# Kernel optimization log

Measured on AMD Instinct MI355X. Metric: run time of the kernel, lower is better.

## Reference

```python
import jax, jax.numpy as jnp
import numpy as np

N, DX, DS, NLAB, NSMAT = 20000, 16, 64, 10, 64
E_HALF = 160000
E = 2 * E_HALF
N_LABELED = 2000
N_HIDDEN = 6  # six Linear(nsmat,nsmat) layers between input and output layers


def setup_inputs() -> dict:
    key = jax.random.key(0)
    ks = jax.random.split(key, 16)
    xembed = jax.random.normal(ks[0], (N, DX), jnp.float32)
    sembed = jax.random.normal(ks[1], (N, DS), jnp.float32)
    # ylprob are log-probabilities (original uses exp(ylprob) in the KL term)
    ylprob = jax.nn.log_softmax(jax.random.normal(ks[2], (N, NLAB), jnp.float32), axis=1)
    # build edge list with explicit reverse pairs so loss_orth is exercised
    s_half = jax.random.randint(ks[3], (E_HALF,), 0, N, jnp.int32)
    t_half = jax.random.randint(ks[4], (E_HALF,), 0, N, jnp.int32)
    src = jnp.concatenate([s_half, t_half])
    tgt = jnp.concatenate([t_half, s_half])
    edge_w = jax.random.uniform(ks[5], (E,), jnp.float32, 0.1, 1.0)
    rev1 = jnp.arange(E_HALF, dtype=jnp.int32)
    rev2 = rev1 + E_HALF
    idvert = jax.random.randint(ks[6], (N_LABELED,), 0, N, jnp.int32)
    fcW_in = jax.random.normal(ks[7], (2 * DS, NSMAT), jnp.float32) / np.sqrt(2 * DS)
    fcb_in = jnp.zeros((NSMAT,), jnp.float32)
    fcW_h = jax.random.normal(ks[8], (N_HIDDEN, NSMAT, NSMAT), jnp.float32) / np.sqrt(NSMAT)
    fcb_h = jnp.zeros((N_HIDDEN, NSMAT), jnp.float32)
    fcW_out = jax.random.normal(ks[9], (NSMAT, DX * DX), jnp.float32) / np.sqrt(NSMAT)
    fcb_out = jnp.zeros((DX * DX,), jnp.float32)
    # cl_smat params: Linear(dimx, nlab) + LogSoftmax
    clW = jax.random.normal(ks[10], (DX, NLAB), jnp.float32) / np.sqrt(DX)
    clb = jnp.zeros((NLAB,), jnp.float32)
    return dict(xembed=xembed, sembed=sembed, ylprob=ylprob, edge_w=edge_w,
                fcW_in=fcW_in, fcb_in=fcb_in, fcW_h=fcW_h, fcb_h=fcb_h,
                fcW_out=fcW_out, fcb_out=fcb_out, clW=clW, clb=clb,
                src=src, tgt=tgt, rev1=rev1, rev2=rev2, idvert=idvert)


def _edge_matrices(sf, tf, fcW_in, fcb_in, fcW_h, fcb_h, fcW_out, fcb_out):
    # [E, 2*dims] -> 8-layer ReLU MLP -> [E, dimx, dimx]
    h = jax.nn.relu(jnp.concatenate([sf, tf], axis=1) @ fcW_in + fcb_in)
    for i in range(N_HIDDEN):
        h = jax.nn.relu(h @ fcW_h[i] + fcb_h[i])
    return (h @ fcW_out + fcb_out).reshape(-1, DX, DX)


def reference(xembed, sembed, ylprob, edge_w, fcW_in, fcb_in, fcW_h, fcb_h,
              fcW_out, fcb_out, clW, clb, src, tgt, rev1, rev2, idvert):
    # per-edge sheaf transport matrices from gathered structure embeddings
    edge_mats = _edge_matrices(sembed[src], sembed[tgt],
                               fcW_in, fcb_in, fcW_h, fcb_h, fcW_out, fcb_out)

    # orthogonality loss over reverse edge pairs: mean RMS(A@B - I) * dimx
    prod = jnp.einsum('eij,ejk->eik', edge_mats[rev1], edge_mats[rev2])
    diff = prod - jnp.eye(DX, dtype=prod.dtype)
    loss_orth = jnp.mean(jnp.sqrt(jnp.mean(diff * diff, axis=(1, 2)) * (DX * DX)))

    # message passing: gather -> bmm -> weighted scatter-add -> degree normalize
    messages = jnp.einsum('eij,ej->ei', edge_mats, xembed[src])  # [E, dimx]
    weighted = messages * edge_w[:, None]
    new_x = jax.ops.segment_sum(weighted, tgt, num_segments=N)   # [N, dimx]
    deg = jax.ops.segment_sum(edge_w, tgt, num_segments=N)       # [N]
    xmaped = jnp.where((deg > 0)[:, None], new_x / jnp.maximum(deg, 1e-20)[:, None], new_x)

    loss_smap = jnp.mean((xmaped - xembed) ** 2) * DX

    # KL(y || g) on labeled nodes; cl_smat = Linear + LogSoftmax
    glprob = jax.nn.log_softmax(xmaped[idvert] @ clW + clb, axis=1)
    ylp = ylprob[idvert]
    loss_lbpr = jnp.mean(jnp.sum(jnp.exp(ylp) * (ylp - glprob), axis=1))

    # original recomputes the same MLP on the same inputs and takes the MSE of
    # two identical tensors -> exactly zero (and zero gradient)
    loss_cons = jnp.zeros((), xembed.dtype)

    return (loss_orth, loss_cons, loss_smap, loss_lbpr)
```

## Files before the change

### kernel.cpp

```cpp
#include <hip/hip_runtime.h>
#include <hip/hip_bf16.h>

#define N_NODES   20000
#define DX        16
#define DS        64
#define NLAB      10
#define NSMAT     64
#define E_HALF    160000
#define E_TOT     320000
#define N_LABELED 2000
#define N_HIDDEN  6

#define PAIRS 32
#define NT    (E_HALF / PAIRS)

typedef short bf16x8 __attribute__((ext_vector_type(8)));
typedef float f32x4  __attribute__((ext_vector_type(4)));
#define MFMA16(a, b, c) __builtin_amdgcn_mfma_f32_16x16x32_bf16((a), (b), (c), 0, 0, 0)

#define LDS_A0    0
#define LDS_H0    16384
#define LDS_H1    24576
#define LDS_MT    32768
#define LDS_X     49152
#define LDS_BH    51200
#define LDS_BOUT  52736
#define LDS_TOTAL 53760

#define WS_W0     0
#define WS_WH     16384
#define WS_WOUT   65536
#define WS_FLOATS 98304

__device__ __forceinline__ unsigned short f2bf(float f) {
    unsigned int u = __float_as_uint(f);
    unsigned int r = (u + 0x7fffu + ((u >> 16) & 1u)) >> 16;
    return (unsigned short)r;
}
__device__ __forceinline__ unsigned int packbf(float a, float b) {
    return (unsigned int)f2bf(a) | ((unsigned int)f2bf(b) << 16);
}
__device__ __forceinline__ float bflo(unsigned int u) { return __uint_as_float(u << 16); }
__device__ __forceinline__ float bfhi(unsigned int u) { return __uint_as_float(u & 0xffff0000u); }

__global__ void k_prep(const float* __restrict__ Win, const float* __restrict__ Wh,
                       const float* __restrict__ Wout, unsigned short* __restrict__ wsw) {
    const int idx = blockIdx.x * 256 + threadIdx.x;
    if (idx >= 49152) return;
    float val; int base, KK, k, n;
    if (idx < 8192) {
        k = idx >> 6; n = idx & 63; val = Win[idx]; base = WS_W0 / 2; KK = 4;
    } else if (idx < 32768) {
        const int r = idx - 8192; const int l = r >> 12; const int rr = r & 4095;
        k = rr >> 6; n = rr & 63; val = Wh[r]; base = (WS_WH + l * 8192) / 2; KK = 2;
    } else {
        const int r = idx - 32768; k = r >> 8; n = r & 255;
        val = Wout[r]; base = WS_WOUT / 2; KK = 2;
    }
    const int ntile = n >> 4, kk = k >> 5, hi = (k >> 3) & 3, j = k & 7;
    const int lane = hi * 16 + (n & 15);
    wsw[base + (((ntile * KK + kk) * 64 + lane) * 8 + j)] = f2bf(val);
}

__global__ void k_zero(float* __restrict__ p, int n) {
    int i = blockIdx.x * blockDim.x + threadIdx.x;
    const int stride = gridDim.x * blockDim.x;
    for (; i < n; i += stride) p[i] = 0.0f;
}

__global__ __launch_bounds__(256, 3) void k_main(
    const float* __restrict__ xembed, const float* __restrict__ sembed,
    const float* __restrict__ edge_w,
    const float* __restrict__ bin, const float* __restrict__ bh,
    const float* __restrict__ bout,
    const int* __restrict__ src, const int* __restrict__ tgt,
    const unsigned short* __restrict__ wsw,
    float* __restrict__ newx, float* __restrict__ deg,
    float* __restrict__ orth_part)
{
    extern __shared__ char lds[];
    const int tid    = threadIdx.x;
    const int lane   = tid & 63;
    const int wv     = tid >> 6;
    const int lane15 = lane & 15;
    const int hi     = lane >> 4;
    const int p0     = blockIdx.x * PAIRS;

    if (tid < 96)       ((float4*)(lds + LDS_BH))[tid]       = ((const float4*)bh)[tid];
    else if (tid < 160) ((float4*)(lds + LDS_BOUT))[tid - 96] = ((const float4*)bout)[tid - 96];

    {
        const int si = tid >> 3, sc = tid & 7;
        const bool sT = (sc >= 4); const int scc = sc & 3;
        const int p = p0 + si;
        const int nodeA = sT ? tgt[p] : src[p];
        const float4* nrow = (const float4*)(sembed + (size_t)nodeA * DS + scc * 16);
        const float4 v0 = nrow[0], v1 = nrow[1], v2 = nrow[2], v3 = nrow[3];
        const int colA = (sT ? 128 : 0) + scc * 32;
        const int colB = (sT ? 0 : 128) + scc * 32;
        const int sXor = (si & 7) << 4;
        uint2 pk;
        pk.x = packbf(v0.x, v0.y); pk.y = packbf(v0.z, v0.w);
        *(uint2*)(lds + LDS_A0 + si * 256 + ((colA + 0) ^ sXor)) = pk;
        *(uint2*)(lds + LDS_A0 + (32 + si) * 256 + ((colB + 0) ^ sXor)) = pk;
        pk.x = packbf(v1.x, v1.y); pk.y = packbf(v1.z, v1.w);
        *(uint2*)(lds + LDS_A0 + si * 256 + ((colA + 8) ^ sXor)) = pk;
        *(uint2*)(lds + LDS_A0 + (32 + si) * 256 + ((colB + 8) ^ sXor)) = pk;
        pk.x = packbf(v2.x, v2.y); pk.y = packbf(v2.z, v2.w);
        *(uint2*)(lds + LDS_A0 + si * 256 + ((colA + 16) ^ sXor)) = pk;
        *(uint2*)(lds + LDS_A0 + (32 + si) * 256 + ((colB + 16) ^ sXor)) = pk;
        pk.x = packbf(v3.x, v3.y); pk.y = packbf(v3.z, v3.w);
        *(uint2*)(lds + LDS_A0 + si * 256 + ((colA + 24) ^ sXor)) = pk;
        *(uint2*)(lds + LDS_A0 + (32 + si) * 256 + ((colB + 24) ^ sXor)) = pk;

        const int sed = tid >> 2, sqq = tid & 3;
        const int nodeX = (sed < 32) ? src[p0 + sed] : tgt[p0 + sed - 32];
        const float4 vx = *(const float4*)(xembed + (size_t)nodeX * DX + sqq * 4);
        pk.x = packbf(vx.x, vx.y); pk.y = packbf(vx.z, vx.w);
        *(uint2*)(lds + LDS_X + sed * 32 + sqq * 8) = pk;
    }

    float bin_r[4];
    #pragma unroll
    for (int n = 0; n < 4; ++n) bin_r[n] = bin[16 * n + lane15];

    const int arow = 16 * wv + lane15;
    const int axor = (arow & 7) << 4;

    __syncthreads();

    {
        bf16x8 a[4];
        #pragma unroll
        for (int kk = 0; kk < 4; ++kk)
            a[kk] = *(const bf16x8*)(lds + LDS_A0 + arow * 256 + ((kk * 64 + hi * 16) ^ axor));
        const unsigned short* w0g = wsw + WS_W0 / 2;
        #pragma unroll
        for (int n = 0; n < 4; ++n) {
            f32x4 acc = {bin_r[n], bin_r[n], bin_r[n], bin_r[n]};
            #pragma unroll
            for (int kk = 0; kk < 4; ++kk) {
                const bf16x8 b = *(const bf16x8*)(w0g + ((n * 4 + kk) * 64 + lane) * 8);
                acc = MFMA16(a[kk], b, acc);
            }
            #pragma unroll
            for (int r = 0; r < 4; ++r) {
                const int row = 16 * wv + 4 * hi + r;
                *(unsigned short*)(lds + LDS_H0 + row * 128 +
                    (((16 * n + lane15) * 2) ^ ((row & 7) << 4))) = f2bf(fmaxf(acc[r], 0.0f));
            }
        }
    }
    __syncthreads();

    #pragma unroll
    for (int l = 0; l < 6; ++l) {
        const int sB = (l & 1) ? LDS_H1 : LDS_H0;
        const int dB = (l & 1) ? LDS_H0 : LDS_H1;
        const unsigned short* whg = wsw + WS_WH / 2 + l * 4096;
        const bf16x8 a0 = *(const bf16x8*)(lds + sB + arow * 128 + ((hi * 16) ^ axor));
        const bf16x8 a1 = *(const bf16x8*)(lds + sB + arow * 128 + ((64 + hi * 16) ^ axor));
        #pragma unroll
        for (int n = 0; n < 4; ++n) {
            const float bv = ((const float*)(lds + LDS_BH))[l * 64 + 16 * n + lane15];
            f32x4 acc = {bv, bv, bv, bv};
            const bf16x8 b0 = *(const bf16x8*)(whg + ((n * 2 + 0) * 64 + lane) * 8);
            const bf16x8 b1 = *(const bf16x8*)(whg + ((n * 2 + 1) * 64 + lane) * 8);
            acc = MFMA16(a0, b0, acc);
            acc = MFMA16(a1, b1, acc);
            #pragma unroll
            for (int r = 0; r < 4; ++r) {
                const int row = 16 * wv + 4 * hi + r;
                *(unsigned short*)(lds + dB + row * 128 +
                    (((16 * n + lane15) * 2) ^ ((row & 7) << 4))) = f2bf(fmaxf(acc[r], 0.0f));
            }
        }
    }

    {
        const bf16x8 a0 = *(const bf16x8*)(lds + LDS_H0 + arow * 128 + ((hi * 16) ^ axor));
        const bf16x8 a1 = *(const bf16x8*)(lds + LDS_H0 + arow * 128 + ((64 + hi * 16) ^ axor));
        const unsigned short* wog = wsw + WS_WOUT / 2;
        #pragma unroll
        for (int n = 0; n < 16; ++n) {
            const float bv = ((const float*)(lds + LDS_BOUT))[16 * n + lane15];
            const bf16x8 b0 = *(const bf16x8*)(wog + ((n * 2 + 0) * 64 + lane) * 8);
            const bf16x8 b1 = *(const bf16x8*)(wog + ((n * 2 + 1) * 64 + lane) * 8);
            f32x4 acc = {bv, bv, bv, bv};
            acc = MFMA16(a0, b0, acc);
            acc = MFMA16(a1, b1, acc);
            #pragma unroll
            for (int r = 0; r < 4; ++r) {
                const int row = 16 * wv + 4 * hi + r;
                const unsigned short mv = f2bf(acc[r]);
                if (wv < 2) {
                    const int i = row;
                    *(unsigned short*)(lds + LDS_A0 + i * 512 +
                        (((n * 16 + lane15) * 2) ^ ((i & 7) << 4))) = mv;
                } else {
                    const int i = row - 32;
                    *(unsigned short*)(lds + LDS_MT + i * 512 +
                        (((lane15 * 16 + n) * 2) ^ ((i & 7) << 4))) = mv;
                }
            }
        }
    }
    __syncthreads();

    {
        const int e = tid >> 2, q = tid & 3;
        const int i = e & 31;
        const bool isB = (e >= 32);
        const uint4 x0 = *(const uint4*)(lds + LDS_X + e * 32);
        const uint4 x1 = *(const uint4*)(lds + LDS_X + e * 32 + 16);
        float xv[16];
        xv[0]  = bflo(x0.x); xv[1]  = bfhi(x0.x); xv[2]  = bflo(x0.y); xv[3]  = bfhi(x0.y);
        xv[4]  = bflo(x0.z); xv[5]  = bfhi(x0.z); xv[6]  = bflo(x0.w); xv[7]  = bfhi(x0.w);
        xv[8]  = bflo(x1.x); xv[9]  = bfhi(x1.x); xv[10] = bflo(x1.y); xv[11] = bfhi(x1.y);
        xv[12] = bflo(x1.z); xv[13] = bfhi(x1.z); xv[14] = bflo(x1.w); xv[15] = bfhi(x1.w);
        const int p = p0 + i;
        const float w_e  = isB ? edge_w[p + E_HALF] : edge_w[p];
        const int target = isB ? src[p] : tgt[p];
        const int ixor = (i & 7) << 4;
        if (!isB) {
            #pragma unroll
            for (int jj = 0; jj < 4; ++jj) {
                const int row = 4 * q + jj;
                const uint4 m0 = *(const uint4*)(lds + LDS_A0 + i * 512 + ((row * 32) ^ ixor));
                const uint4 m1 = *(const uint4*)(lds + LDS_A0 + i * 512 + ((row * 32 + 16) ^ ixor));
                float m = bflo(m0.x) * xv[0];
                m = fmaf(bfhi(m0.x), xv[1], m);  m = fmaf(bflo(m0.y), xv[2], m);
                m = fmaf(bfhi(m0.y), xv[3], m);  m = fmaf(bflo(m0.z), xv[4], m);
                m = fmaf(bfhi(m0.z), xv[5], m);  m = fmaf(bflo(m0.w), xv[6], m);
                m = fmaf(bfhi(m0.w), xv[7], m);  m = fmaf(bflo(m1.x), xv[8], m);
                m = fmaf(bfhi(m1.x), xv[9], m);  m = fmaf(bflo(m1.y), xv[10], m);
                m = fmaf(bfhi(m1.y), xv[11], m); m = fmaf(bflo(m1.z), xv[12], m);
                m = fmaf(bfhi(m1.z), xv[13], m); m = fmaf(bflo(m1.w), xv[14], m);
                m = fmaf(bfhi(m1.w), xv[15], m);
                atomicAdd(&newx[(size_t)target * DX + row], w_e * m);
            }
        } else {
            float macc[4] = {0.f, 0.f, 0.f, 0.f};
            #pragma unroll
            for (int c = 0; c < 16; ++c) {
                const uint2 v = *(const uint2*)(lds + LDS_MT + i * 512 + ((c * 32 + q * 8) ^ ixor));
                const float xc = xv[c];
                macc[0] = fmaf(bflo(v.x), xc, macc[0]);
                macc[1] = fmaf(bfhi(v.x), xc, macc[1]);
                macc[2] = fmaf(bflo(v.y), xc, macc[2]);
                macc[3] = fmaf(bfhi(v.y), xc, macc[3]);
            }
            #pragma unroll
            for (int jj = 0; jj < 4; ++jj)
                atomicAdd(&newx[(size_t)target * DX + 4 * q + jj], w_e * macc[jj]);
        }
        if (q == 0) atomicAdd(&deg[target], w_e);
    }

    float wsum = 0.0f;
    {
        const bf16x8 zf = {0, 0, 0, 0, 0, 0, 0, 0};
        #pragma unroll
        for (int pp = 0; pp < 8; ++pp) {
            const int pi = 8 * wv + pp;
            const int pxor = (pi & 7) << 4;
            const int off = (lane15 * 32 + (hi & 1) * 16) ^ pxor;
            bf16x8 af  = *(const bf16x8*)(lds + LDS_A0 + pi * 512 + off);
            bf16x8 bfr = *(const bf16x8*)(lds + LDS_MT + pi * 512 + off);
            if (hi >= 2) { af = zf; bfr = zf; }
            f32x4 pr = {0.f, 0.f, 0.f, 0.f};
            pr = MFMA16(af, bfr, pr);
            float ss = 0.0f;
            #pragma unroll
            for (int r = 0; r < 4; ++r) {
                const float d = pr[r] - ((4 * hi + r == lane15) ? 1.0f : 0.0f);
                ss = fmaf(d, d, ss);
            }
            #pragma unroll
            for (int o = 32; o > 0; o >>= 1) ss += __shfl_xor(ss, o, 64);
            wsum += sqrtf(ss);
        }
    }
    __syncthreads();
    if (lane == 0) ((float*)(lds + LDS_BH))[wv] = wsum;
    __syncthreads();
    if (tid == 0) {
        const float* pw = (const float*)(lds + LDS_BH);
        atomicAdd(&orth_part[blockIdx.x & 255], pw[0] + pw[1] + pw[2] + pw[3]);
    }
}

__device__ __forceinline__ float block_reduce_256(float v) {
    __shared__ float part[4];
    #pragma unroll
    for (int off = 32; off > 0; off >>= 1) v += __shfl_xor(v, off, 64);
    const int lane = threadIdx.x & 63, wid = threadIdx.x >> 6;
    if (lane == 0) part[wid] = v;
    __syncthreads();
    float s = 0.0f;
    if (threadIdx.x == 0) {
        #pragma unroll
        for (int i = 0; i < 4; ++i) s += part[i];
    }
    return s;
}

__global__ __launch_bounds__(256) void k_smap(
    const float* __restrict__ xembed, float* __restrict__ nx,
    const float* __restrict__ deg, float* __restrict__ accum)
{
    const int n = blockIdx.x * 256 + threadIdx.x;
    float ss = 0.0f;
    if (n < N_NODES) {
        const float d = deg[n];
        const float inv = 1.0f / fmaxf(d, 1e-20f);
        #pragma unroll
        for (int c = 0; c < DX; ++c) {
            const float v  = nx[(size_t)n * DX + c];
            const float xm = (d > 0.0f) ? v * inv : v;
            nx[(size_t)n * DX + c] = xm;
            const float df = xm - xembed[(size_t)n * DX + c];
            ss = fmaf(df, df, ss);
        }
    }
    ss = block_reduce_256(ss);
    if (threadIdx.x == 0) atomicAdd(&accum[1], ss);
}

__global__ __launch_bounds__(256) void k_lbpr(
    const float* __restrict__ ylprob, const float* __restrict__ xmaped,
    const float* __restrict__ clW, const float* __restrict__ clb,
    const int* __restrict__ idvert, float* __restrict__ accum)
{
    const int v = blockIdx.x * 256 + threadIdx.x;
    float kl = 0.0f;
    if (v < N_LABELED) {
        const int n = idvert[v];
        float z[NLAB];
        #pragma unroll
        for (int c = 0; c < NLAB; ++c) z[c] = clb[c];
        #pragma unroll
        for (int i = 0; i < DX; ++i) {
            const float xi = xmaped[(size_t)n * DX + i];
            #pragma unroll
            for (int c = 0; c < NLAB; ++c) z[c] = fmaf(xi, clW[i * NLAB + c], z[c]);
        }
        float mx = z[0];
        #pragma unroll
        for (int c = 1; c < NLAB; ++c) mx = fmaxf(mx, z[c]);
        float se = 0.0f;
        #pragma unroll
        for (int c = 0; c < NLAB; ++c) se += expf(z[c] - mx);
        const float lse = mx + logf(se);
        #pragma unroll
        for (int c = 0; c < NLAB; ++c) {
            const float yl = ylprob[(size_t)n * NLAB + c];
            kl += expf(yl) * (yl - (z[c] - lse));
        }
    }
    kl = block_reduce_256(kl);
    if (threadIdx.x == 0) atomicAdd(&accum[2], kl);
}

__global__ __launch_bounds__(256) void k_final(
    const float* __restrict__ accum, const float* __restrict__ orth_part,
    float* __restrict__ out)
{
    float v = orth_part[threadIdx.x];
    v = block_reduce_256(v);
    if (threadIdx.x == 0) {
        out[0] = v * (1.0f / (float)E_HALF);
        out[1] = 0.0f;
        out[2] = accum[1] * (1.0f / (float)N_NODES);
        out[3] = accum[2] * (1.0f / (float)N_LABELED);
    }
}

extern "C" void kernel_launch(void* const* d_in, const int* in_sizes, int n_in,
                              void* d_out, int out_size, void* d_ws, size_t ws_size,
                              hipStream_t stream) {
    const float* xembed = (const float*)d_in[0];
    const float* sembed = (const float*)d_in[1];
    const float* ylprob = (const float*)d_in[2];
    const float* edge_w = (const float*)d_in[3];
    const float* Win    = (const float*)d_in[4];
    const float* bin    = (const float*)d_in[5];
    const float* Wh     = (const float*)d_in[6];
    const float* bh     = (const float*)d_in[7];
    const float* Wout   = (const float*)d_in[8];
    const float* bout   = (const float*)d_in[9];
    const float* clW    = (const float*)d_in[10];
    const float* clb    = (const float*)d_in[11];
    const int*   src    = (const int*)d_in[12];
    const int*   tgt    = (const int*)d_in[13];
    const int*   idvert = (const int*)d_in[16];

    unsigned short* wsw = (unsigned short*)d_ws;
    float* wsF       = (float*)((char*)d_ws + WS_FLOATS);
    float* newx      = wsF;
    float* deg       = wsF + (size_t)N_NODES * DX;
    float* accum     = deg + N_NODES;
    float* orth_part = accum + 4;
    const int nzero = N_NODES * DX + N_NODES + 4 + 256;

    k_prep<<<192, 256, 0, stream>>>(Win, Wh, Wout, wsw);
    k_zero<<<512, 256, 0, stream>>>(wsF, nzero);

    k_main<<<NT, 256, LDS_TOTAL, stream>>>(
        xembed, sembed, edge_w, bin, bh, bout, src, tgt, wsw, newx, deg, orth_part);

    k_smap<<<(N_NODES + 255) / 256, 256, 0, stream>>>(xembed, newx, deg, accum);
    k_lbpr<<<(N_LABELED + 255) / 256, 256, 0, stream>>>(ylprob, newx, clW, clb, idvert, accum);
    k_final<<<1, 256, 0, stream>>>(accum, orth_part, (float*)d_out);
}
```

Measured before the change: 151.5 us.

## Shrink LDS footprint, keep biases and x in registers, raise occupancy to 4 blocks

Biases are now held in registers instead of LDS, and the gathered x rows are kept in registers and shared across lanes with shuffles, so they are no longer staged through LDS. The MT buffer is overlapped with the H1 region, which cuts LDS from about 53KB to 40KB, and launch bounds are raised to 4 blocks per CU. Bf16 packing now uses the hardware v_cvt_pk_bf16_f32 instruction, and a barrier is added before the output layer. The trade-off is higher register pressure from roughly 44 extra bias registers under a tighter per-thread register limit, which may cause spills. Reusing the H1 region for MT also relies on the newly added barrier to be correct.

```diff
diff --git a/kernel.cpp b/kernel.cpp
--- a/kernel.cpp
+++ b/kernel.cpp
@@ -21,11 +21,8 @@
 #define LDS_A0    0
 #define LDS_H0    16384
 #define LDS_H1    24576
-#define LDS_MT    32768
-#define LDS_X     49152
-#define LDS_BH    51200
-#define LDS_BOUT  52736
-#define LDS_TOTAL 53760
+#define LDS_MT    24576
+#define LDS_TOTAL 40960
 
 #define WS_W0     0
 #define WS_WH     16384
@@ -37,8 +34,10 @@
     unsigned int r = (u + 0x7fffu + ((u >> 16) & 1u)) >> 16;
     return (unsigned short)r;
 }
-__device__ __forceinline__ unsigned int packbf(float a, float b) {
-    return (unsigned int)f2bf(a) | ((unsigned int)f2bf(b) << 16);
+__device__ __forceinline__ unsigned int cvtpk(float lo, float hi) {
+    unsigned int r;
+    asm("v_cvt_pk_bf16_f32 %0, %1, %2" : "=v"(r) : "v"(lo), "v"(hi));
+    return r;
 }
 __device__ __forceinline__ float bflo(unsigned int u) { return __uint_as_float(u << 16); }
 __device__ __forceinline__ float bfhi(unsigned int u) { return __uint_as_float(u & 0xffff0000u); }
@@ -68,7 +67,7 @@
     for (; i < n; i += stride) p[i] = 0.0f;
 }
 
-__global__ __launch_bounds__(256, 3) void k_main(
+__global__ __launch_bounds__(256, 4) void k_main(
     const float* __restrict__ xembed, const float* __restrict__ sembed,
     const float* __restrict__ edge_w,
     const float* __restrict__ bin, const float* __restrict__ bh,
@@ -86,9 +85,18 @@
     const int hi     = lane >> 4;
     const int p0     = blockIdx.x * PAIRS;
 
-    if (tid < 96)       ((float4*)(lds + LDS_BH))[tid]       = ((const float4*)bh)[tid];
-    else if (tid < 160) ((float4*)(lds + LDS_BOUT))[tid - 96] = ((const float4*)bout)[tid - 96];
-
+    float bin_r[4], bh_r[N_HIDDEN][4], bout_r[16];
+    #pragma unroll
+    for (int n = 0; n < 4; ++n) bin_r[n] = bin[16 * n + lane15];
+    #pragma unroll
+    for (int l = 0; l < N_HIDDEN; ++l) {
+        #pragma unroll
+        for (int n = 0; n < 4; ++n) bh_r[l][n] = bh[l * 64 + 16 * n + lane15];
+    }
+    #pragma unroll
+    for (int n = 0; n < 16; ++n) bout_r[n] = bout[16 * n + lane15];
+
+    float4 sx;
     {
         const int si = tid >> 3, sc = tid & 7;
         const bool sT = (sc >= 4); const int scc = sc & 3;
@@ -100,29 +108,23 @@
         const int colB = (sT ? 0 : 128) + scc * 32;
         const int sXor = (si & 7) << 4;
         uint2 pk;
-        pk.x = packbf(v0.x, v0.y); pk.y = packbf(v0.z, v0.w);
+        pk.x = cvtpk(v0.x, v0.y); pk.y = cvtpk(v0.z, v0.w);
         *(uint2*)(lds + LDS_A0 + si * 256 + ((colA + 0) ^ sXor)) = pk;
         *(uint2*)(lds + LDS_A0 + (32 + si) * 256 + ((colB + 0) ^ sXor)) = pk;
-        pk.x = packbf(v1.x, v1.y); pk.y = packbf(v1.z, v1.w);
+        pk.x = cvtpk(v1.x, v1.y); pk.y = cvtpk(v1.z, v1.w);
         *(uint2*)(lds + LDS_A0 + si * 256 + ((colA + 8) ^ sXor)) = pk;
         *(uint2*)(lds + LDS_A0 + (32 + si) * 256 + ((colB + 8) ^ sXor)) = pk;
-        pk.x = packbf(v2.x, v2.y); pk.y = packbf(v2.z, v2.w);
+        pk.x = cvtpk(v2.x, v2.y); pk.y = cvtpk(v2.z, v2.w);
         *(uint2*)(lds + LDS_A0 + si * 256 + ((colA + 16) ^ sXor)) = pk;
         *(uint2*)(lds + LDS_A0 + (32 + si) * 256 + ((colB + 16) ^ sXor)) = pk;
-        pk.x = packbf(v3.x, v3.y); pk.y = packbf(v3.z, v3.w);
+        pk.x = cvtpk(v3.x, v3.y); pk.y = cvtpk(v3.z, v3.w);
         *(uint2*)(lds + LDS_A0 + si * 256 + ((colA + 24) ^ sXor)) = pk;
         *(uint2*)(lds + LDS_A0 + (32 + si) * 256 + ((colB + 24) ^ sXor)) = pk;
 
         const int sed = tid >> 2, sqq = tid & 3;
         const int nodeX = (sed < 32) ? src[p0 + sed] : tgt[p0 + sed - 32];
-        const float4 vx = *(const float4*)(xembed + (size_t)nodeX * DX + sqq * 4);
-        pk.x = packbf(vx.x, vx.y); pk.y = packbf(vx.z, vx.w);
-        *(uint2*)(lds + LDS_X + sed * 32 + sqq * 8) = pk;
-    }
-
-    float bin_r[4];
-    #pragma unroll
-    for (int n = 0; n < 4; ++n) bin_r[n] = bin[16 * n + lane15];
+        sx = *(const float4*)(xembed + (size_t)nodeX * DX + sqq * 4);
+    }
 
     const int arow = 16 * wv + lane15;
     const int axor = (arow & 7) << 4;
@@ -146,15 +148,16 @@
             #pragma unroll
             for (int r = 0; r < 4; ++r) {
                 const int row = 16 * wv + 4 * hi + r;
-                *(unsigned short*)(lds + LDS_H0 + row * 128 +
-                    (((16 * n + lane15) * 2) ^ ((row & 7) << 4))) = f2bf(fmaxf(acc[r], 0.0f));
+                *(__hip_bfloat16*)(lds + LDS_H0 + row * 128 +
+                    (((16 * n + lane15) * 2) ^ ((row & 7) << 4))) =
+                    __float2bfloat16(fmaxf(acc[r], 0.0f));
             }
         }
     }
     __syncthreads();
 
     #pragma unroll
-    for (int l = 0; l < 6; ++l) {
+    for (int l = 0; l < N_HIDDEN; ++l) {
         const int sB = (l & 1) ? LDS_H1 : LDS_H0;
         const int dB = (l & 1) ? LDS_H0 : LDS_H1;
         const unsigned short* whg = wsw + WS_WH / 2 + l * 4096;
@@ -162,8 +165,7 @@
         const bf16x8 a1 = *(const bf16x8*)(lds + sB + arow * 128 + ((64 + hi * 16) ^ axor));
         #pragma unroll
         for (int n = 0; n < 4; ++n) {
-            const float bv = ((const float*)(lds + LDS_BH))[l * 64 + 16 * n + lane15];
-            f32x4 acc = {bv, bv, bv, bv};
+            f32x4 acc = {bh_r[l][n], bh_r[l][n], bh_r[l][n], bh_r[l][n]};
             const bf16x8 b0 = *(const bf16x8*)(whg + ((n * 2 + 0) * 64 + lane) * 8);
             const bf16x8 b1 = *(const bf16x8*)(whg + ((n * 2 + 1) * 64 + lane) * 8);
             acc = MFMA16(a0, b0, acc);
@@ -171,11 +173,13 @@
             #pragma unroll
             for (int r = 0; r < 4; ++r) {
                 const int row = 16 * wv + 4 * hi + r;
-                *(unsigned short*)(lds + dB + row * 128 +
-                    (((16 * n + lane15) * 2) ^ ((row & 7) << 4))) = f2bf(fmaxf(acc[r], 0.0f));
-            }
-        }
-    }
+                *(__hip_bfloat16*)(lds + dB + row * 128 +
+                    (((16 * n + lane15) * 2) ^ ((row & 7) << 4))) =
+                    __float2bfloat16(fmaxf(acc[r], 0.0f));
+            }
+        }
+    }
+    __syncthreads();
 
     {
         const bf16x8 a0 = *(const bf16x8*)(lds + LDS_H0 + arow * 128 + ((hi * 16) ^ axor));
@@ -183,23 +187,22 @@
         const unsigned short* wog = wsw + WS_WOUT / 2;
         #pragma unroll
         for (int n = 0; n < 16; ++n) {
-            const float bv = ((const float*)(lds + LDS_BOUT))[16 * n + lane15];
             const bf16x8 b0 = *(const bf16x8*)(wog + ((n * 2 + 0) * 64 + lane) * 8);
             const bf16x8 b1 = *(const bf16x8*)(wog + ((n * 2 + 1) * 64 + lane) * 8);
-            f32x4 acc = {bv, bv, bv, bv};
+            f32x4 acc = {bout_r[n], bout_r[n], bout_r[n], bout_r[n]};
             acc = MFMA16(a0, b0, acc);
             acc = MFMA16(a1, b1, acc);
             #pragma unroll
             for (int r = 0; r < 4; ++r) {
                 const int row = 16 * wv + 4 * hi + r;
-                const unsigned short mv = f2bf(acc[r]);
+                const __hip_bfloat16 mv = __float2bfloat16(acc[r]);
                 if (wv < 2) {
                     const int i = row;
-                    *(unsigned short*)(lds + LDS_A0 + i * 512 +
+                    *(__hip_bfloat16*)(lds + LDS_A0 + i * 512 +
                         (((n * 16 + lane15) * 2) ^ ((i & 7) << 4))) = mv;
                 } else {
                     const int i = row - 32;
-                    *(unsigned short*)(lds + LDS_MT + i * 512 +
+                    *(__hip_bfloat16*)(lds + LDS_MT + i * 512 +
                         (((lane15 * 16 + n) * 2) ^ ((i & 7) << 4))) = mv;
                 }
             }
@@ -211,13 +214,14 @@
         const int e = tid >> 2, q = tid & 3;
         const int i = e & 31;
         const bool isB = (e >= 32);
-        const uint4 x0 = *(const uint4*)(lds + LDS_X + e * 32);
-        const uint4 x1 = *(const uint4*)(lds + LDS_X + e * 32 + 16);
         float xv[16];
-        xv[0]  = bflo(x0.x); xv[1]  = bfhi(x0.x); xv[2]  = bflo(x0.y); xv[3]  = bfhi(x0.y);
-        xv[4]  = bflo(x0.z); xv[5]  = bfhi(x0.z); xv[6]  = bflo(x0.w); xv[7]  = bfhi(x0.w);
-        xv[8]  = bflo(x1.x); xv[9]  = bfhi(x1.x); xv[10] = bflo(x1.y); xv[11] = bfhi(x1.y);
-        xv[12] = bflo(x1.z); xv[13] = bfhi(x1.z); xv[14] = bflo(x1.w); xv[15] = bfhi(x1.w);
+        #pragma unroll
+        for (int qq = 0; qq < 4; ++qq) {
+            xv[4 * qq + 0] = __shfl(sx.x, qq, 4);
+            xv[4 * qq + 1] = __shfl(sx.y, qq, 4);
+            xv[4 * qq + 2] = __shfl(sx.z, qq, 4);
+            xv[4 * qq + 3] = __shfl(sx.w, qq, 4);
+        }
         const int p = p0 + i;
         const float w_e  = isB ? edge_w[p + E_HALF] : edge_w[p];
         const int target = isB ? src[p] : tgt[p];
@@ -282,10 +286,10 @@
         }
     }
     __syncthreads();
-    if (lane == 0) ((float*)(lds + LDS_BH))[wv] = wsum;
+    if (lane == 0) ((float*)(lds + LDS_A0))[wv] = wsum;
     __syncthreads();
     if (tid == 0) {
-        const float* pw = (const float*)(lds + LDS_BH);
+        const float* pw = (const float*)(lds + LDS_A0);
         atomicAdd(&orth_part[blockIdx.x & 255], pw[0] + pw[1] + pw[2] + pw[3]);
     }
 }
```

Result: slower. 189.5 us (+25.1%).
